# Kernel optimization log

Hardware: AMD Instinct MI355X
Metric: run time of the kernel (lower is better)

Reference implementation:

```python
import jax, jax.numpy as jnp
import numpy as np

N_NODES = 128
N_EDGES = N_NODES * (N_NODES - 1)  # fully-connected, no self-loops
N_IN = 128
N_HID = 256
N_OUT = 128
BATCH = 32


def _build_rel_matrices():
    # one-hot incidence matrices for fully-connected off-diagonal graph
    send_idx, recv_idx = [], []
    for i in range(N_NODES):
        for j in range(N_NODES):
            if i != j:
                send_idx.append(i)
                recv_idx.append(j)
    eye = np.eye(N_NODES, dtype=np.float32)
    rel_send = eye[np.asarray(send_idx)]  # [E, N]
    rel_rec = eye[np.asarray(recv_idx)]   # [E, N]
    return jnp.asarray(rel_rec), jnp.asarray(rel_send)


def setup_inputs() -> dict:
    key = jax.random.key(0)
    k = jax.random.split(key, 6)
    rel_rec, rel_send = _build_rel_matrices()
    s1 = 1.0 / np.sqrt(2 * N_IN)
    s2 = 1.0 / np.sqrt(N_HID)
    return {
        "x": jax.random.normal(k[0], (BATCH, N_NODES, N_IN), dtype=jnp.float32),
        "rel_type": jax.random.uniform(k[1], (BATCH, N_EDGES, 4), dtype=jnp.float32),
        "rel_rec": rel_rec,
        "rel_send": rel_send,
        "W1": jax.random.normal(k[2], (2 * N_IN, N_HID), dtype=jnp.float32) * s1,
        "b1": jnp.zeros((N_HID,), dtype=jnp.float32),
        "W2": jax.random.normal(k[3], (N_HID, N_OUT), dtype=jnp.float32) * s2,
        "b2": jnp.zeros((N_OUT,), dtype=jnp.float32),
    }


def reference(x, rel_type, rel_rec, rel_send, W1, b1, W2, b2):
    # node2edge: gather sender/receiver node features via incidence matmuls
    senders = jnp.einsum('en,bnf->bef', rel_send, x)    # [B, E, n_in]
    receivers = jnp.einsum('en,bnf->bef', rel_rec, x)   # [B, E, n_in]
    edges = jnp.concatenate([senders, receivers], axis=-1)  # [B, E, 2*n_in]
    # 2-layer MLP on edges (rel_type is unused in the original forward)
    h = jax.nn.relu(edges @ W1 + b1)
    msg = h @ W2 + b2                                   # [B, E, n_out]
    # edge2node: scatter-sum then normalize by in-degree
    agg = jnp.einsum('en,bef->bnf', rel_rec, msg)       # [B, N, n_out]
    norm = rel_rec.sum(axis=0)[None, :, None]           # [1, N, 1]
    return agg / (norm + 1e-6)
```

## Files before the change

### kernel.cpp

```cpp
#include <hip/hip_runtime.h>

#define BATCH 32
#define NN    128
#define NIN   128
#define NHID  256
#define NOUT  128
#define ROWS  (BATCH * NN)

typedef __attribute__((ext_vector_type(2))) float f32x2;

__global__ __launch_bounds__(512) void k1_sr(
    const float* __restrict__ x, const float* __restrict__ W1,
    const float* __restrict__ b1, float* __restrict__ S, float* __restrict__ R)
{
    __shared__ float xr[16][128];
    const int row0 = blockIdx.x * 16;
    const int t = threadIdx.x;

    ((float4*)xr)[t] = ((const float4*)(x + (size_t)row0 * NIN))[t];
    __syncthreads();

    const int c  = t & 255;
    const int rh = t >> 8;

    f32x2 accs[8], accr[8];
#pragma unroll
    for (int r = 0; r < 8; ++r) { accs[r] = (f32x2)0.f; accr[r] = (f32x2)0.f; }

    for (int k = 0; k < NIN; k += 4) {
        f32x2 wa0, wa1, wb0, wb1;
        wa0.x = W1[(size_t)(k+0)*NHID + c]; wa0.y = W1[(size_t)(k+1)*NHID + c];
        wa1.x = W1[(size_t)(k+2)*NHID + c]; wa1.y = W1[(size_t)(k+3)*NHID + c];
        wb0.x = W1[(size_t)(NIN+k+0)*NHID + c]; wb0.y = W1[(size_t)(NIN+k+1)*NHID + c];
        wb1.x = W1[(size_t)(NIN+k+2)*NHID + c]; wb1.y = W1[(size_t)(NIN+k+3)*NHID + c];
#pragma unroll
        for (int r = 0; r < 8; ++r) {
            const float4 xv = *(const float4*)(&xr[rh * 8 + r][k]);
            f32x2 xlo; xlo.x = xv.x; xlo.y = xv.y;
            f32x2 xhi; xhi.x = xv.z; xhi.y = xv.w;
            accs[r] = __builtin_elementwise_fma(xlo, wa0, accs[r]);
            accs[r] = __builtin_elementwise_fma(xhi, wa1, accs[r]);
            accr[r] = __builtin_elementwise_fma(xlo, wb0, accr[r]);
            accr[r] = __builtin_elementwise_fma(xhi, wb1, accr[r]);
        }
    }
    const float bias = b1[c];
#pragma unroll
    for (int r = 0; r < 8; ++r) {
        const int row = row0 + rh * 8 + r;
        S[(size_t)row * NHID + c] = accs[r].x + accs[r].y;
        R[(size_t)row * NHID + c] = accr[r].x + accr[r].y + bias;
    }
}

__global__ __launch_bounds__(512) void k2_fused(
    const float* __restrict__ S, const float* __restrict__ R,
    const float* __restrict__ W2, const float* __restrict__ b2,
    float* __restrict__ out)
{
    __shared__ float sS[128 * 256];
    __shared__ float sG[16 * 256];

    const int blk = blockIdx.x;
    const int b   = blk >> 3;
    const int nt  = blk & 7;
    const int n0  = nt * 16;

    const int t = threadIdx.x;
    const int c = t & 255;
    const int h = t >> 8;
    const int r0 = n0 + h * 8;

    float rv[8];
#pragma unroll
    for (int q = 0; q < 8; ++q)
        rv[q] = R[((size_t)(b * NN + r0 + q)) * NHID + c];

    const float4* Sv  = (const float4*)(S + (size_t)b * NN * NHID);
    float4*       sm4 = (float4*)sS;
#pragma unroll
    for (int it = 0; it < 16; ++it)
        sm4[t + it * 512] = Sv[t + it * 512];
    __syncthreads();

    f32x2 rv2[4], aab[4];
#pragma unroll
    for (int j = 0; j < 4; ++j) {
        rv2[j].x = rv[2*j]; rv2[j].y = rv[2*j+1];
        aab[j] = (f32x2)0.f;
    }
    float ssum = 0.f;

#pragma unroll 4
    for (int i = 0; i < NN; ++i) {
        const float s = sS[i * NHID + c];
        ssum += s;
        f32x2 s2; s2.x = s; s2.y = s;
#pragma unroll
        for (int j = 0; j < 4; ++j) {
            const f32x2 tj = s2 + rv2[j];
            aab[j].x += __builtin_fabsf(tj.x);
            aab[j].y += __builtin_fabsf(tj.y);
        }
    }

#pragma unroll
    for (int q = 0; q < 8; ++q) {
        const float aa   = (q & 1) ? aab[q >> 1].y : aab[q >> 1].x;
        const float self = fmaxf(sS[(r0 + q) * NHID + c] + rv[q], 0.f);
        sG[(h * 8 + q) * NHID + c] = 0.5f * (ssum + 128.f * rv[q] + aa) - self;
    }
    __syncthreads();

    const int co = t & 127;
    const int rg = t >> 7;
    f32x2 a2[4];
#pragma unroll
    for (int r = 0; r < 4; ++r) a2[r] = (f32x2)0.f;

    for (int k = 0; k < NHID; k += 4) {
        f32x2 w0, w1;
        w0.x = W2[(size_t)(k+0)*NOUT + co]; w0.y = W2[(size_t)(k+1)*NOUT + co];
        w1.x = W2[(size_t)(k+2)*NOUT + co]; w1.y = W2[(size_t)(k+3)*NOUT + co];
#pragma unroll
        for (int r = 0; r < 4; ++r) {
            const float4 gv = *(const float4*)(&sG[(rg * 4 + r) * NHID + k]);
            f32x2 glo; glo.x = gv.x; glo.y = gv.y;
            f32x2 ghi; ghi.x = gv.z; ghi.y = gv.w;
            a2[r] = __builtin_elementwise_fma(glo, w0, a2[r]);
            a2[r] = __builtin_elementwise_fma(ghi, w1, a2[r]);
        }
    }
    const float inv  = 1.0f / (127.0f + 1e-6f);
    const float bias = 127.0f * b2[co];
#pragma unroll
    for (int r = 0; r < 4; ++r)
        out[((size_t)(b * NN + n0 + rg * 4 + r)) * NOUT + co] =
            (a2[r].x + a2[r].y + bias) * inv;
}

extern "C" void kernel_launch(void* const* d_in, const int* in_sizes, int n_in,
                              void* d_out, int out_size, void* d_ws, size_t ws_size,
                              hipStream_t stream)
{
    const float* x  = (const float*)d_in[0];
    const float* W1 = (const float*)d_in[4];
    const float* b1 = (const float*)d_in[5];
    const float* W2 = (const float*)d_in[6];
    const float* b2 = (const float*)d_in[7];
    float* out = (float*)d_out;

    float* S = (float*)d_ws;
    float* R = S + (size_t)ROWS * NHID;

    k1_sr   <<<ROWS / 16, 512, 0, stream>>>(x, W1, b1, S, R);
    k2_fused<<<BATCH * 8, 512, 0, stream>>>(S, R, W2, b2, out);
}
```

Measured before the change: 114.2 us.

## Merge both kernels into one cooperative kernel with grid-wide sync

Fuses the first-layer projection kernel and the fused aggregation/MLP kernel into a single cooperative launch of 256 blocks. A grid-wide barrier separates producing S/R from consuming them, and block indexing is remapped so each block handles one batch slice in both phases. The aim is to remove the second kernel launch and its gap. In exchange it adds the cost of a grid sync and needs all 256 blocks, each using about 144KB of shared memory, to be co-resident.

```diff
diff --git a/kernel.cpp b/kernel.cpp
--- a/kernel.cpp
+++ b/kernel.cpp
@@ -1,4 +1,7 @@
 #include <hip/hip_runtime.h>
+#include <hip/hip_cooperative_groups.h>
+
+namespace cg = cooperative_groups;
 
 #define BATCH 32
 #define NN    128
@@ -9,66 +12,65 @@
 
 typedef __attribute__((ext_vector_type(2))) float f32x2;
 
-__global__ __launch_bounds__(512) void k1_sr(
+__global__ __launch_bounds__(512) void fused_all(
     const float* __restrict__ x, const float* __restrict__ W1,
-    const float* __restrict__ b1, float* __restrict__ S, float* __restrict__ R)
-{
-    __shared__ float xr[16][128];
-    const int row0 = blockIdx.x * 16;
-    const int t = threadIdx.x;
-
-    ((float4*)xr)[t] = ((const float4*)(x + (size_t)row0 * NIN))[t];
-    __syncthreads();
-
-    const int c  = t & 255;
-    const int rh = t >> 8;
-
-    f32x2 accs[8], accr[8];
-#pragma unroll
-    for (int r = 0; r < 8; ++r) { accs[r] = (f32x2)0.f; accr[r] = (f32x2)0.f; }
-
-    for (int k = 0; k < NIN; k += 4) {
-        f32x2 wa0, wa1, wb0, wb1;
-        wa0.x = W1[(size_t)(k+0)*NHID + c]; wa0.y = W1[(size_t)(k+1)*NHID + c];
-        wa1.x = W1[(size_t)(k+2)*NHID + c]; wa1.y = W1[(size_t)(k+3)*NHID + c];
-        wb0.x = W1[(size_t)(NIN+k+0)*NHID + c]; wb0.y = W1[(size_t)(NIN+k+1)*NHID + c];
-        wb1.x = W1[(size_t)(NIN+k+2)*NHID + c]; wb1.y = W1[(size_t)(NIN+k+3)*NHID + c];
-#pragma unroll
-        for (int r = 0; r < 8; ++r) {
-            const float4 xv = *(const float4*)(&xr[rh * 8 + r][k]);
-            f32x2 xlo; xlo.x = xv.x; xlo.y = xv.y;
-            f32x2 xhi; xhi.x = xv.z; xhi.y = xv.w;
-            accs[r] = __builtin_elementwise_fma(xlo, wa0, accs[r]);
-            accs[r] = __builtin_elementwise_fma(xhi, wa1, accs[r]);
-            accr[r] = __builtin_elementwise_fma(xlo, wb0, accr[r]);
-            accr[r] = __builtin_elementwise_fma(xhi, wb1, accr[r]);
-        }
-    }
-    const float bias = b1[c];
-#pragma unroll
-    for (int r = 0; r < 8; ++r) {
-        const int row = row0 + rh * 8 + r;
-        S[(size_t)row * NHID + c] = accs[r].x + accs[r].y;
-        R[(size_t)row * NHID + c] = accr[r].x + accr[r].y + bias;
-    }
-}
-
-__global__ __launch_bounds__(512) void k2_fused(
-    const float* __restrict__ S, const float* __restrict__ R,
-    const float* __restrict__ W2, const float* __restrict__ b2,
-    float* __restrict__ out)
+    const float* __restrict__ b1, const float* __restrict__ W2,
+    const float* __restrict__ b2, float* __restrict__ S,
+    float* __restrict__ R, float* __restrict__ out)
 {
     __shared__ float sS[128 * 256];
     __shared__ float sG[16 * 256];
 
     const int blk = blockIdx.x;
-    const int b   = blk >> 3;
-    const int nt  = blk & 7;
-    const int n0  = nt * 16;
+    const int t   = threadIdx.x;
+    const int b   = blk & 31;
+    const int j   = blk >> 5;
 
-    const int t = threadIdx.x;
-    const int c = t & 255;
-    const int h = t >> 8;
+    {
+        float* xr = sS;
+        const int row0 = b * NN + j * 16;
+
+        ((float4*)xr)[t] = ((const float4*)(x + (size_t)row0 * NIN))[t];
+        __syncthreads();
+
+        const int c  = t & 255;
+        const int rh = t >> 8;
+
+        f32x2 accs[8], accr[8];
+#pragma unroll
+        for (int r = 0; r < 8; ++r) { accs[r] = (f32x2)0.f; accr[r] = (f32x2)0.f; }
+
+        for (int k = 0; k < NIN; k += 4) {
+            f32x2 wa0, wa1, wb0, wb1;
+            wa0.x = W1[(size_t)(k+0)*NHID + c]; wa0.y = W1[(size_t)(k+1)*NHID + c];
+            wa1.x = W1[(size_t)(k+2)*NHID + c]; wa1.y = W1[(size_t)(k+3)*NHID + c];
+            wb0.x = W1[(size_t)(NIN+k+0)*NHID + c]; wb0.y = W1[(size_t)(NIN+k+1)*NHID + c];
+            wb1.x = W1[(size_t)(NIN+k+2)*NHID + c]; wb1.y = W1[(size_t)(NIN+k+3)*NHID + c];
+#pragma unroll
+            for (int r = 0; r < 8; ++r) {
+                const float4 xv = *(const float4*)(&xr[(rh * 8 + r) * NIN + k]);
+                f32x2 xlo; xlo.x = xv.x; xlo.y = xv.y;
+                f32x2 xhi; xhi.x = xv.z; xhi.y = xv.w;
+                accs[r] = __builtin_elementwise_fma(xlo, wa0, accs[r]);
+                accs[r] = __builtin_elementwise_fma(xhi, wa1, accs[r]);
+                accr[r] = __builtin_elementwise_fma(xlo, wb0, accr[r]);
+                accr[r] = __builtin_elementwise_fma(xhi, wb1, accr[r]);
+            }
+        }
+        const float bias = b1[c];
+#pragma unroll
+        for (int r = 0; r < 8; ++r) {
+            const int row = row0 + rh * 8 + r;
+            S[(size_t)row * NHID + c] = accs[r].x + accs[r].y;
+            R[(size_t)row * NHID + c] = accr[r].x + accr[r].y + bias;
+        }
+    }
+
+    cg::this_grid().sync();
+
+    const int n0 = j * 16;
+    const int c  = t & 255;
+    const int h  = t >> 8;
     const int r0 = n0 + h * 8;
 
     float rv[8];
@@ -76,18 +78,20 @@
     for (int q = 0; q < 8; ++q)
         rv[q] = R[((size_t)(b * NN + r0 + q)) * NHID + c];
 
-    const float4* Sv  = (const float4*)(S + (size_t)b * NN * NHID);
-    float4*       sm4 = (float4*)sS;
+    {
+        const float4* Sv  = (const float4*)(S + (size_t)b * NN * NHID);
+        float4*       sm4 = (float4*)sS;
 #pragma unroll
-    for (int it = 0; it < 16; ++it)
-        sm4[t + it * 512] = Sv[t + it * 512];
+        for (int it = 0; it < 16; ++it)
+            sm4[t + it * 512] = Sv[t + it * 512];
+    }
     __syncthreads();
 
     f32x2 rv2[4], aab[4];
 #pragma unroll
-    for (int j = 0; j < 4; ++j) {
-        rv2[j].x = rv[2*j]; rv2[j].y = rv[2*j+1];
-        aab[j] = (f32x2)0.f;
+    for (int jj = 0; jj < 4; ++jj) {
+        rv2[jj].x = rv[2*jj]; rv2[jj].y = rv[2*jj+1];
+        aab[jj] = (f32x2)0.f;
     }
     float ssum = 0.f;
 
@@ -97,10 +101,10 @@
         ssum += s;
         f32x2 s2; s2.x = s; s2.y = s;
 #pragma unroll
-        for (int j = 0; j < 4; ++j) {
-            const f32x2 tj = s2 + rv2[j];
-            aab[j].x += __builtin_fabsf(tj.x);
-            aab[j].y += __builtin_fabsf(tj.y);
+        for (int jj = 0; jj < 4; ++jj) {
+            const f32x2 tj = s2 + rv2[jj];
+            aab[jj].x += __builtin_fabsf(tj.x);
+            aab[jj].y += __builtin_fabsf(tj.y);
         }
     }
 
@@ -153,6 +157,8 @@
     float* S = (float*)d_ws;
     float* R = S + (size_t)ROWS * NHID;
 
-    k1_sr   <<<ROWS / 16, 512, 0, stream>>>(x, W1, b1, S, R);
-    k2_fused<<<BATCH * 8, 512, 0, stream>>>(S, R, W2, b2, out);
+    void* args[] = { (void*)&x, (void*)&W1, (void*)&b1, (void*)&W2,
+                     (void*)&b2, (void*)&S, (void*)&R, (void*)&out };
+    hipLaunchCooperativeKernel((const void*)fused_all, dim3(256), dim3(512),
+                               args, 0, stream);
 }
```

Result: slower. 161.5 us (+41.5%).
